# Kernel optimization log

Hardware: AMD Instinct MI355X
Metric: run time of the kernel (lower is better)

Reference implementation:

```python
import jax, jax.numpy as jnp
import numpy as np

B, T, IDIM, ODIM, HDIM = 4, 64, 64, 64, 64
THETAS = np.linspace(0.8, 1.2, 5)


def _argaug(x_dis, y):
    """Grid search over scale thetas and all time shifts; keep best cosine-sim window.
    x_dis: (B,T,H,O) key; y: (B,T,idim) query. Returns (x_aug:(B,T,H,idim), sim:(B,T,H))."""
    Bq, Tq, H, O = x_dis.shape
    idim = y.shape[-1]
    qnorm = jnp.linalg.norm(y, axis=-1)  # (B,T)
    best_sim = None
    best_win = None
    for theta in THETAS:
        L = int(np.floor(O * theta))
        # torch F.interpolate mode='nearest': src = floor(dst * in/out)
        src = np.floor(np.arange(L) * (O / L)).astype(np.int32)
        src = np.clip(src, 0, O - 1)
        x_s = x_dis[..., src]  # (B,T,H,L)
        pad = idim - 1
        xp = jnp.pad(x_s, ((0, 0), (0, 0), (0, 0), (pad, pad)))
        S = L + idim - 1  # number of shifts kept by _pad_for_shift
        win_idx = np.arange(S)[:, None] + np.arange(idim)[None, :]  # (S, idim)
        windows = xp[..., win_idx]  # (B,T,H,S,idim)
        dots = jnp.einsum('bthsi,bti->bths', windows, y)
        wnorm = jnp.linalg.norm(windows, axis=-1)  # (B,T,H,S)
        denom = qnorm[:, :, None, None] * wnorm
        safe = jnp.where(denom > 0, denom, 1.0)
        sim = jnp.where(denom > 0, dots / safe, 0.0)  # nan (0/0) -> 0 as in torch
        sim_max = jnp.max(sim, axis=-1)               # (B,T,H)
        idxm = jnp.argmax(sim, axis=-1)               # first max, like torch.max
        opt = jnp.take_along_axis(windows, idxm[..., None, None], axis=3)[..., 0, :]
        if best_sim is None:
            best_sim, best_win = sim_max, opt
        else:
            m = best_sim < sim_max
            best_win = jnp.where(m[..., None], opt, best_win)
            best_sim = jnp.where(m, sim_max, best_sim)
    return best_win, best_sim


def setup_inputs() -> dict:
    key = jax.random.key(0)
    ks = jax.random.split(key, 6)
    x = jax.random.normal(ks[0], (B, T, IDIM), dtype=jnp.float32)
    y = jax.random.normal(ks[1], (B, T, IDIM), dtype=jnp.float32)
    # freq_mask: Bernoulli per hdim channel with Gaussian-kernel prob (sigma=430)
    w = np.exp(-0.5 * (np.arange(HDIM, dtype=np.float32) / 430.0) ** 2)
    w = w / w.max()
    mask = (jax.random.uniform(ks[2], (B, T, HDIM)) < jnp.asarray(w)).astype(jnp.int32)
    xav = 0.1
    W1 = jax.random.normal(ks[3], (HDIM, IDIM), dtype=jnp.float32) * xav
    W2 = jax.random.normal(ks[4], (ODIM, HDIM), dtype=jnp.float32) * xav
    b1 = jnp.zeros((HDIM,), dtype=jnp.float32)
    b2 = jnp.zeros((ODIM,), dtype=jnp.float32)
    return {"x": x, "y": y, "mask": mask, "W1": W1, "b1": b1, "W2": W2, "b2": b2}


def reference(x, y, mask, W1, b1, W2, b2):
    # h = fc1(x) * mask
    h = jnp.einsum('bti,hi->bth', x, W1) + b1
    h = h * mask.astype(h.dtype)
    # disentangle: fc2(eye*h) -> per-channel rank-1 outputs (B,T,H,O)
    x_dis = jnp.einsum('bth,oh->btho', h, W2) + b2
    # argaug grid search
    x_aug, sim_max_global = _argaug(x_dis, y)  # (B,T,H,idim)
    # h = fc1(x_aug); out = sum_H fc2(h)
    h2 = jnp.einsum('bthi,ji->bthj', x_aug, W1) + b1
    out = jnp.einsum('bthj,oj->btho', h2, W2) + b2
    out = jnp.sum(out, axis=-2)  # (B,T,O)
    xf = out.reshape(-1, out.shape[-1])
    yf = y.reshape(-1, y.shape[-1])
    m = yf == 0.0  # ignore_out = 0.0 (not NaN)
    denom = jnp.sum(~m).astype(xf.dtype)
    loss = jnp.sum(jnp.where(m, 0.0, (xf - yf) ** 2)) / denom
    return loss, xf
```

## Files before the change

### kernel.cpp

```cpp
#include <hip/hip_runtime.h>
#include <math.h>

#define NT 512
#define NWAVE 8

__global__ __launch_bounds__(NT) void argaug_scan(
    const float* __restrict__ x, const float* __restrict__ y,
    const int* __restrict__ mask,
    const float* __restrict__ W1, const float* __restrict__ b1,
    const float* __restrict__ W2, const float* __restrict__ b2,
    double* __restrict__ outN, double* __restrict__ outD, int* __restrict__ outS)
{
    __shared__ double wdBuf[76 * 64];
    __shared__ double ypad[80];
    __shared__ float  sx[64], sh[64], sb1[64];

    double* rsimN = wdBuf;
    double* rsimD = wdBuf + NWAVE * 64;
    int*    ridxB = (int*)(wdBuf + 2 * NWAVE * 64);

    const int tid = threadIdx.x;
    const int bx  = blockIdx.x;
    const int bt  = bx & 255;
    const int t5  = bx >> 8;
    const int hh  = tid & 63;
    const int sg  = tid >> 6;

    const double theta = (t5 == 4) ? 1.2 : (0.8 + (double)t5 * ((1.2 - 0.8) / 4.0));
    const int L = (int)floor(64.0 * theta);
    const int S = L + 63;
    const double rcp = 64.0 / (double)L;

    if (tid < 64) {
        sx[tid]  = x[bt * 64 + tid];
        sb1[tid] = b1[tid];
    } else if (tid >= 128 && tid < 208) {
        const int p = tid - 128;
        ypad[p] = (p >= 8 && p < 72) ? (double)y[bt * 64 + p - 8] : 0.0;
    }
    __syncthreads();

    if (tid < 64) {
        float acc = 0.0f;
        const float* w1r = W1 + tid * 64;
        for (int i = 0; i < 64; ++i) acc = fmaf(sx[i], w1r[i], acc);
        acc += sb1[tid];
        sh[tid] = acc * (float)mask[bt * 64 + tid];
    }
    __syncthreads();

    for (int k = tid; k < L * 64; k += NT) {
        const int j = k >> 6, h = k & 63;
        int sj = (int)floor((double)j * rcp);
        if (sj > 63) sj = 63;
        const float wf = fmaf(sh[h], W2[sj * 64 + h], b2[sj]);
        wdBuf[k] = (double)wf;
    }
    __syncthreads();

    double bN = -1.0, bD = 0.0; int bi = 0x7fffffff;
    #pragma unroll 2
    for (int pp = 0; pp < 2; ++pp) {
        const int s_first = 9 * (sg + 8 * pp);
        if (s_first >= S) continue;
        const int jstart = (s_first > 63) ? (s_first - 63) : 0;
        const int jmid   = (s_first < L - 1) ? s_first : (L - 1);
        const int jend   = (s_first + 8 < L - 1) ? (s_first + 8) : (L - 1);
        const int C      = 71 - s_first;

        double d0=0,d1=0,d2=0,d3=0,d4=0,d5=0,d6=0,d7=0,d8=0,ssA=0;
        double ym1 = ypad[jstart + C - 1];
        double ym2 = ypad[jstart + C - 2];
        double ym3 = ypad[jstart + C - 3];
        double ym4 = ypad[jstart + C - 4];
        double ym5 = ypad[jstart + C - 5];
        double ym6 = ypad[jstart + C - 6];
        double ym7 = ypad[jstart + C - 7];
        double ym8 = ypad[jstart + C - 8];

        #pragma unroll 9
        for (int j = jstart; j <= jmid; ++j) {
            const double w  = wdBuf[j * 64 + hh];
            const double y0 = ypad[j + C];
            d0 = fma(w, y0,  d0); d1 = fma(w, ym1, d1); d2 = fma(w, ym2, d2);
            d3 = fma(w, ym3, d3); d4 = fma(w, ym4, d4); d5 = fma(w, ym5, d5);
            d6 = fma(w, ym6, d6); d7 = fma(w, ym7, d7); d8 = fma(w, ym8, d8);
            ssA = fma(w, w, ssA);
            ym8=ym7; ym7=ym6; ym6=ym5; ym5=ym4; ym4=ym3; ym3=ym2; ym2=ym1; ym1=y0;
        }
        #pragma unroll 9
        for (int j = jmid + 1; j <= jend; ++j) {
            const double w  = wdBuf[j * 64 + hh];
            const double y0 = ypad[j + C];
            d0 = fma(w, y0,  d0); d1 = fma(w, ym1, d1); d2 = fma(w, ym2, d2);
            d3 = fma(w, ym3, d3); d4 = fma(w, ym4, d4); d5 = fma(w, ym5, d5);
            d6 = fma(w, ym6, d6); d7 = fma(w, ym7, d7); d8 = fma(w, ym8, d8);
            ym8=ym7; ym7=ym6; ym6=ym5; ym5=ym4; ym4=ym3; ym3=ym2; ym2=ym1; ym1=y0;
        }

        const int kmax = (S - s_first < 9) ? (S - s_first) : 9;
        double ss = ssA;
        #define SSUP(kk) { \
            const int jh = s_first + kk; \
            const int jl = jh - 64; \
            if (jh <= L - 1) { const double w = wdBuf[jh * 64 + hh]; ss = fma(w,  w, ss); } \
            if (jl >= 0)     { const double w = wdBuf[jl * 64 + hh]; ss = fma(-w, w, ss); } }
        #define EVALK(kk, dk) { \
            double pn, pd; \
            if (ss > 0.0) { pn = dk * fabs(dk); pd = ss; } \
            else          { pn = 0.0;           pd = 1.0; } \
            if (pn * bD > bN * pd) { bN = pn; bD = pd; bi = s_first + kk; } }
        EVALK(0, d0)
        if (1 < kmax) { SSUP(1) EVALK(1, d1) }
        if (2 < kmax) { SSUP(2) EVALK(2, d2) }
        if (3 < kmax) { SSUP(3) EVALK(3, d3) }
        if (4 < kmax) { SSUP(4) EVALK(4, d4) }
        if (5 < kmax) { SSUP(5) EVALK(5, d5) }
        if (6 < kmax) { SSUP(6) EVALK(6, d6) }
        if (7 < kmax) { SSUP(7) EVALK(7, d7) }
        if (8 < kmax) { SSUP(8) EVALK(8, d8) }
        #undef SSUP
        #undef EVALK
    }

    __syncthreads();
    rsimN[sg * 64 + hh] = bN;
    rsimD[sg * 64 + hh] = bD;
    ridxB[sg * 64 + hh] = bi;
    __syncthreads();
    if (tid < 64) {
        double mN = -1.0, mD = 0.0; int mi = 0x7fffffff;
        for (int g = 0; g < NWAVE; ++g) {
            const double vN = rsimN[g * 64 + tid];
            const double vD = rsimD[g * 64 + tid];
            const int    vi = ridxB[g * 64 + tid];
            const double a = vN * mD, b = mN * vD;
            if (a > b || (a == b && vi < mi)) { mN = vN; mD = vD; mi = vi; }
        }
        const int o = bx * 64 + tid;
        outN[o] = mN;
        outD[o] = mD;
        outS[o] = mi;
    }
}

__global__ __launch_bounds__(256) void merge_epilogue(
    const float* __restrict__ x, const float* __restrict__ y,
    const int* __restrict__ mask,
    const float* __restrict__ W1, const float* __restrict__ b1,
    const float* __restrict__ W2, const float* __restrict__ b2,
    const double* __restrict__ N, const double* __restrict__ D,
    const int* __restrict__ S,
    float* __restrict__ xf, double* __restrict__ psum, double* __restrict__ pcnt)
{
    __shared__ float  sx[64], sy[64], sh[64];
    __shared__ int    bS[64], bT[64];
    __shared__ double part[4][64], ssum[64], su[64];

    const int tid = threadIdx.x;
    const int bt  = blockIdx.x;
    const int g   = tid >> 6, i = tid & 63;

    if (tid < 64) {
        sx[tid] = x[bt * 64 + tid];
        sy[tid] = y[bt * 64 + tid];
    }
    __syncthreads();
    if (tid < 64) {
        float acc = 0.0f;
        const float* w1r = W1 + tid * 64;
        for (int k = 0; k < 64; ++k) acc = fmaf(sx[k], w1r[k], acc);
        acc += b1[tid];
        sh[tid] = acc * (float)mask[bt * 64 + tid];
        double mN = -1.0, mD = 0.0; int mS = 0, mT = 0;
        for (int t5 = 0; t5 < 5; ++t5) {
            const int o = (t5 * 256 + bt) * 64 + tid;
            const double vN = N[o], vD = D[o];
            if (vN * mD > mN * vD) { mN = vN; mD = vD; mS = S[o]; mT = t5; }
        }
        bS[tid] = mS; bT[tid] = mT;
    }
    __syncthreads();

    {
        double acc = 0.0;
        for (int q = 0; q < 16; ++q) {
            const int h = g * 16 + q;
            const int t5 = bT[h];
            const double theta = (t5 == 4) ? 1.2 : (0.8 + (double)t5 * ((1.2 - 0.8) / 4.0));
            const int L = (int)floor(64.0 * theta);
            const double rcp = 64.0 / (double)L;
            const int j = bS[h] - 63 + i;
            if (j >= 0 && j < L) {
                int sj = (int)floor((double)j * rcp);
                if (sj > 63) sj = 63;
                acc += (double)fmaf(sh[h], W2[sj * 64 + h], b2[sj]);
            }
        }
        part[g][i] = acc;
    }
    __syncthreads();
    if (tid < 64) {
        ssum[tid] = part[0][tid] + part[1][tid] + part[2][tid] + part[3][tid];
    }
    __syncthreads();
    {
        double acc = 0.0;
        const int base = g * 16;
        for (int q = 0; q < 16; ++q)
            acc += (double)W1[i * 64 + base + q] * ssum[base + q];
        part[g][i] = acc;
    }
    __syncthreads();
    if (tid < 64) {
        su[tid] = 64.0 * (double)b1[tid]
                + part[0][tid] + part[1][tid] + part[2][tid] + part[3][tid];
    }
    __syncthreads();
    {
        double acc = 0.0;
        const int base = g * 16;
        for (int q = 0; q < 16; ++q)
            acc += (double)W2[i * 64 + base + q] * su[base + q];
        part[g][i] = acc;
    }
    __syncthreads();
    if (tid < 64) {
        const double v = 64.0 * (double)b2[tid]
                       + part[0][tid] + part[1][tid] + part[2][tid] + part[3][tid];
        const float outf = (float)v;
        xf[bt * 64 + tid] = outf;
        const float yv = sy[tid];
        double pl = 0.0, pc = 0.0;
        if (yv != 0.0f) {
            const float d = outf - yv;
            pl = (double)(d * d);
            pc = 1.0;
        }
        for (int o = 32; o > 0; o >>= 1) {
            pl += __shfl_down(pl, o, 64);
            pc += __shfl_down(pc, o, 64);
        }
        if (tid == 0) { psum[bt] = pl; pcnt[bt] = pc; }
    }
}

__global__ __launch_bounds__(256) void finalize_loss(
    const double* __restrict__ psum, const double* __restrict__ pcnt,
    float* __restrict__ out)
{
    __shared__ double a[256], c[256];
    const int t = threadIdx.x;
    a[t] = psum[t];
    c[t] = pcnt[t];
    __syncthreads();
    for (int s = 128; s > 0; s >>= 1) {
        if (t < s) { a[t] += a[t + s]; c[t] += c[t + s]; }
        __syncthreads();
    }
    if (t == 0) out[0] = (float)(a[0] / c[0]);
}

extern "C" void kernel_launch(void* const* d_in, const int* in_sizes, int n_in,
                              void* d_out, int out_size, void* d_ws, size_t ws_size,
                              hipStream_t stream) {
    const float* x    = (const float*)d_in[0];
    const float* y    = (const float*)d_in[1];
    const int*   mask = (const int*)d_in[2];
    const float* W1   = (const float*)d_in[3];
    const float* b1   = (const float*)d_in[4];
    const float* W2   = (const float*)d_in[5];
    const float* b2   = (const float*)d_in[6];
    float* out = (float*)d_out;

    char* ws = (char*)d_ws;
    double* Nw   = (double*)(ws);
    double* Dw   = (double*)(ws + 655360);
    int*    Sw   = (int*)(ws + 1310720);
    double* psum = (double*)(ws + 1638400);
    double* pcnt = (double*)(ws + 1640448);

    argaug_scan<<<1280, NT, 0, stream>>>(x, y, mask, W1, b1, W2, b2,
                                         Nw, Dw, Sw);
    merge_epilogue<<<256, 256, 0, stream>>>(x, y, mask, W1, b1, W2, b2,
                                            Nw, Dw, Sw,
                                            out + 1, psum, pcnt);
    finalize_loss<<<1, 256, 0, stream>>>(psum, pcnt, out);
}
```

Before: 49.80 us.

## Fuse scan, merge and loss into one kernel with last-block atomic counters

Merges the three kernels into a single launch. Per-(b,t) atomic counters let the last of the five theta blocks run the merge and epilogue, and a global counter lets the last block reduce the loss. Similarity is stored as one quotient instead of a numerator/denominator pair, and the inner loop is rewritten with register rotation macros instead of shift chains. Block-to-(bt,theta) mapping becomes interleaved. It adds a memset launch and atomics/threadfences, and storing the quotient may change tie-breaking slightly.

Measured after the change: 81.91 us. 1.64x slower.

```diff
diff --git a/kernel.cpp b/kernel.cpp
--- a/kernel.cpp
+++ b/kernel.cpp
@@ -2,27 +2,64 @@
 #include <math.h>
 
 #define NT 512
-#define NWAVE 8
-
-__global__ __launch_bounds__(NT) void argaug_scan(
+
+#define BODYS(J, R0,R1,R2,R3,R4,R5,R6,R7,R8) { \
+    const double wv = wdBuf[(J) * 64 + hh]; \
+    R0 = ypad[(J) + C]; \
+    d0 = fma(wv, R0, d0); d1 = fma(wv, R1, d1); d2 = fma(wv, R2, d2); \
+    d3 = fma(wv, R3, d3); d4 = fma(wv, R4, d4); d5 = fma(wv, R5, d5); \
+    d6 = fma(wv, R6, d6); d7 = fma(wv, R7, d7); d8 = fma(wv, R8, d8); \
+    ssq = fma(wv, wv, ssq); }
+
+#define BODYN(J, R0,R1,R2,R3,R4,R5,R6,R7,R8) { \
+    const double wv = wdBuf[(J) * 64 + hh]; \
+    R0 = ypad[(J) + C]; \
+    d0 = fma(wv, R0, d0); d1 = fma(wv, R1, d1); d2 = fma(wv, R2, d2); \
+    d3 = fma(wv, R3, d3); d4 = fma(wv, R4, d4); d5 = fma(wv, R5, d5); \
+    d6 = fma(wv, R6, d6); d7 = fma(wv, R7, d7); d8 = fma(wv, R8, d8); }
+
+#define BS(J, R) BODYS(J, R)
+#define BN(J, R) BODYN(J, R)
+
+#define ROT0 q0,q1,q2,q3,q4,q5,q6,q7,q8
+#define ROT1 q8,q0,q1,q2,q3,q4,q5,q6,q7
+#define ROT2 q7,q8,q0,q1,q2,q3,q4,q5,q6
+#define ROT3 q6,q7,q8,q0,q1,q2,q3,q4,q5
+#define ROT4 q5,q6,q7,q8,q0,q1,q2,q3,q4
+#define ROT5 q4,q5,q6,q7,q8,q0,q1,q2,q3
+#define ROT6 q3,q4,q5,q6,q7,q8,q0,q1,q2
+#define ROT7 q2,q3,q4,q5,q6,q7,q8,q0,q1
+#define ROT8 q1,q2,q3,q4,q5,q6,q7,q8,q0
+
+#define PROLOG(JB) { \
+    q1 = ypad[(JB) + C - 1]; q2 = ypad[(JB) + C - 2]; \
+    q3 = ypad[(JB) + C - 3]; q4 = ypad[(JB) + C - 4]; \
+    q5 = ypad[(JB) + C - 5]; q6 = ypad[(JB) + C - 6]; \
+    q7 = ypad[(JB) + C - 7]; q8 = ypad[(JB) + C - 8]; }
+
+__global__ __launch_bounds__(NT) void argaug_fused(
     const float* __restrict__ x, const float* __restrict__ y,
     const int* __restrict__ mask,
     const float* __restrict__ W1, const float* __restrict__ b1,
     const float* __restrict__ W2, const float* __restrict__ b2,
-    double* __restrict__ outN, double* __restrict__ outD, int* __restrict__ outS)
+    double* __restrict__ simW, int* __restrict__ SwG,
+    double* __restrict__ psum, double* __restrict__ pcnt,
+    int* __restrict__ cnt_bt, int* __restrict__ cnt_all,
+    float* out)
 {
     __shared__ double wdBuf[76 * 64];
     __shared__ double ypad[80];
-    __shared__ float  sx[64], sh[64], sb1[64];
-
-    double* rsimN = wdBuf;
-    double* rsimD = wdBuf + NWAVE * 64;
-    int*    ridxB = (int*)(wdBuf + 2 * NWAVE * 64);
+    __shared__ float  sxy[64];
+    __shared__ float  sh[64], sb1[64];
+    __shared__ int    eflag[2];
+
+    double* rsimQ = wdBuf;
+    int*    ridxB = (int*)(wdBuf + 512);
 
     const int tid = threadIdx.x;
     const int bx  = blockIdx.x;
-    const int bt  = bx & 255;
-    const int t5  = bx >> 8;
+    const int bt  = bx / 5;
+    const int t5  = bx % 5;
     const int hh  = tid & 63;
     const int sg  = tid >> 6;
 
@@ -32,7 +69,7 @@
     const double rcp = 64.0 / (double)L;
 
     if (tid < 64) {
-        sx[tid]  = x[bt * 64 + tid];
+        sxy[tid] = x[bt * 64 + tid];
         sb1[tid] = b1[tid];
     } else if (tid >= 128 && tid < 208) {
         const int p = tid - 128;
@@ -43,7 +80,7 @@
     if (tid < 64) {
         float acc = 0.0f;
         const float* w1r = W1 + tid * 64;
-        for (int i = 0; i < 64; ++i) acc = fmaf(sx[i], w1r[i], acc);
+        for (int i = 0; i < 64; ++i) acc = fmaf(sxy[i], w1r[i], acc);
         acc += sb1[tid];
         sh[tid] = acc * (float)mask[bt * 64 + tid];
     }
@@ -53,13 +90,12 @@
         const int j = k >> 6, h = k & 63;
         int sj = (int)floor((double)j * rcp);
         if (sj > 63) sj = 63;
-        const float wf = fmaf(sh[h], W2[sj * 64 + h], b2[sj]);
-        wdBuf[k] = (double)wf;
+        wdBuf[k] = (double)fmaf(sh[h], W2[sj * 64 + h], b2[sj]);
     }
     __syncthreads();
 
     double bN = -1.0, bD = 0.0; int bi = 0x7fffffff;
-    #pragma unroll 2
+    #pragma unroll 1
     for (int pp = 0; pp < 2; ++pp) {
         const int s_first = 9 * (sg + 8 * pp);
         if (s_first >= S) continue;
@@ -68,38 +104,44 @@
         const int jend   = (s_first + 8 < L - 1) ? (s_first + 8) : (L - 1);
         const int C      = 71 - s_first;
 
-        double d0=0,d1=0,d2=0,d3=0,d4=0,d5=0,d6=0,d7=0,d8=0,ssA=0;
-        double ym1 = ypad[jstart + C - 1];
-        double ym2 = ypad[jstart + C - 2];
-        double ym3 = ypad[jstart + C - 3];
-        double ym4 = ypad[jstart + C - 4];
-        double ym5 = ypad[jstart + C - 5];
-        double ym6 = ypad[jstart + C - 6];
-        double ym7 = ypad[jstart + C - 7];
-        double ym8 = ypad[jstart + C - 8];
-
-        #pragma unroll 9
-        for (int j = jstart; j <= jmid; ++j) {
-            const double w  = wdBuf[j * 64 + hh];
-            const double y0 = ypad[j + C];
-            d0 = fma(w, y0,  d0); d1 = fma(w, ym1, d1); d2 = fma(w, ym2, d2);
-            d3 = fma(w, ym3, d3); d4 = fma(w, ym4, d4); d5 = fma(w, ym5, d5);
-            d6 = fma(w, ym6, d6); d7 = fma(w, ym7, d7); d8 = fma(w, ym8, d8);
-            ssA = fma(w, w, ssA);
-            ym8=ym7; ym7=ym6; ym6=ym5; ym5=ym4; ym4=ym3; ym3=ym2; ym2=ym1; ym1=y0;
-        }
-        #pragma unroll 9
-        for (int j = jmid + 1; j <= jend; ++j) {
-            const double w  = wdBuf[j * 64 + hh];
-            const double y0 = ypad[j + C];
-            d0 = fma(w, y0,  d0); d1 = fma(w, ym1, d1); d2 = fma(w, ym2, d2);
-            d3 = fma(w, ym3, d3); d4 = fma(w, ym4, d4); d5 = fma(w, ym5, d5);
-            d6 = fma(w, ym6, d6); d7 = fma(w, ym7, d7); d8 = fma(w, ym8, d8);
-            ym8=ym7; ym7=ym6; ym6=ym5; ym5=ym4; ym4=ym3; ym3=ym2; ym2=ym1; ym1=y0;
+        double d0=0,d1=0,d2=0,d3=0,d4=0,d5=0,d6=0,d7=0,d8=0,ssq=0;
+        double q0=0,q1,q2,q3,q4,q5,q6,q7,q8;
+
+        int j = jstart;
+        PROLOG(j)
+        const int endA = jmid + 1;
+        while (j + 9 <= endA) {
+            BS(j+0, ROT0) BS(j+1, ROT1) BS(j+2, ROT2)
+            BS(j+3, ROT3) BS(j+4, ROT4) BS(j+5, ROT5)
+            BS(j+6, ROT6) BS(j+7, ROT7) BS(j+8, ROT8)
+            j += 9;
+        }
+        const int remA = endA - j;
+        if (remA > 0) { BS(j+0, ROT0) }
+        if (remA > 1) { BS(j+1, ROT1) }
+        if (remA > 2) { BS(j+2, ROT2) }
+        if (remA > 3) { BS(j+3, ROT3) }
+        if (remA > 4) { BS(j+4, ROT4) }
+        if (remA > 5) { BS(j+5, ROT5) }
+        if (remA > 6) { BS(j+6, ROT6) }
+        if (remA > 7) { BS(j+7, ROT7) }
+
+        const int lenB = jend - jmid;
+        if (lenB > 0) {
+            j = jmid + 1;
+            PROLOG(j)
+            { BN(j+0, ROT0) }
+            if (lenB > 1) { BN(j+1, ROT1) }
+            if (lenB > 2) { BN(j+2, ROT2) }
+            if (lenB > 3) { BN(j+3, ROT3) }
+            if (lenB > 4) { BN(j+4, ROT4) }
+            if (lenB > 5) { BN(j+5, ROT5) }
+            if (lenB > 6) { BN(j+6, ROT6) }
+            if (lenB > 7) { BN(j+7, ROT7) }
         }
 
         const int kmax = (S - s_first < 9) ? (S - s_first) : 9;
-        double ss = ssA;
+        double ss = ssq;
         #define SSUP(kk) { \
             const int jh = s_first + kk; \
             const int jl = jh - 64; \
@@ -124,113 +166,101 @@
     }
 
     __syncthreads();
-    rsimN[sg * 64 + hh] = bN;
-    rsimD[sg * 64 + hh] = bD;
+    rsimQ[sg * 64 + hh] = bN / bD;
     ridxB[sg * 64 + hh] = bi;
     __syncthreads();
     if (tid < 64) {
-        double mN = -1.0, mD = 0.0; int mi = 0x7fffffff;
-        for (int g = 0; g < NWAVE; ++g) {
-            const double vN = rsimN[g * 64 + tid];
-            const double vD = rsimD[g * 64 + tid];
-            const int    vi = ridxB[g * 64 + tid];
-            const double a = vN * mD, b = mN * vD;
-            if (a > b || (a == b && vi < mi)) { mN = vN; mD = vD; mi = vi; }
-        }
-        const int o = bx * 64 + tid;
-        outN[o] = mN;
-        outD[o] = mD;
-        outS[o] = mi;
-    }
-}
-
-__global__ __launch_bounds__(256) void merge_epilogue(
-    const float* __restrict__ x, const float* __restrict__ y,
-    const int* __restrict__ mask,
-    const float* __restrict__ W1, const float* __restrict__ b1,
-    const float* __restrict__ W2, const float* __restrict__ b2,
-    const double* __restrict__ N, const double* __restrict__ D,
-    const int* __restrict__ S,
-    float* __restrict__ xf, double* __restrict__ psum, double* __restrict__ pcnt)
-{
-    __shared__ float  sx[64], sy[64], sh[64];
-    __shared__ int    bS[64], bT[64];
-    __shared__ double part[4][64], ssum[64], su[64];
-
-    const int tid = threadIdx.x;
-    const int bt  = blockIdx.x;
-    const int g   = tid >> 6, i = tid & 63;
-
-    if (tid < 64) {
-        sx[tid] = x[bt * 64 + tid];
-        sy[tid] = y[bt * 64 + tid];
-    }
-    __syncthreads();
-    if (tid < 64) {
-        float acc = 0.0f;
-        const float* w1r = W1 + tid * 64;
-        for (int k = 0; k < 64; ++k) acc = fmaf(sx[k], w1r[k], acc);
-        acc += b1[tid];
-        sh[tid] = acc * (float)mask[bt * 64 + tid];
-        double mN = -1.0, mD = 0.0; int mS = 0, mT = 0;
-        for (int t5 = 0; t5 < 5; ++t5) {
-            const int o = (t5 * 256 + bt) * 64 + tid;
-            const double vN = N[o], vD = D[o];
-            if (vN * mD > mN * vD) { mN = vN; mD = vD; mS = S[o]; mT = t5; }
-        }
-        bS[tid] = mS; bT[tid] = mT;
+        double m = rsimQ[tid]; int mi = ridxB[tid];
+        for (int g = 1; g < 8; ++g) {
+            const double v = rsimQ[g * 64 + tid]; const int vi = ridxB[g * 64 + tid];
+            if (v > m || (v == m && vi < mi)) { m = v; mi = vi; }
+        }
+        const int o = (t5 * 256 + bt) * 64 + tid;
+        simW[o] = m;
+        SwG[o]  = mi;
+    }
+    __syncthreads();
+
+    if (tid == 0) {
+        __threadfence();
+        const int old = atomicAdd(&cnt_bt[bt], 1);
+        if (old == 4) { __threadfence(); eflag[0] = 1; } else eflag[0] = 0;
+    }
+    __syncthreads();
+    if (eflag[0] == 0) return;
+
+    double* mpart = wdBuf;
+    double* mssum = wdBuf + 512;
+    double* msu   = wdBuf + 576;
+    int*    mbS   = (int*)(wdBuf + 640);
+    int*    mbT   = mbS + 64;
+
+    if (tid < 64) {
+        sxy[tid] = y[bt * 64 + tid];
+        int o0 = bt * 64 + tid;
+        double mN = simW[o0]; int mS = SwG[o0], mT = 0;
+        for (int t = 1; t < 5; ++t) {
+            const int o = (t * 256 + bt) * 64 + tid;
+            const double v = simW[o];
+            if (v > mN) { mN = v; mS = SwG[o]; mT = t; }
+        }
+        mbS[tid] = mS; mbT[tid] = mT;
     }
     __syncthreads();
 
     {
+        const int g = sg, i = hh;
         double acc = 0.0;
-        for (int q = 0; q < 16; ++q) {
-            const int h = g * 16 + q;
-            const int t5 = bT[h];
-            const double theta = (t5 == 4) ? 1.2 : (0.8 + (double)t5 * ((1.2 - 0.8) / 4.0));
-            const int L = (int)floor(64.0 * theta);
-            const double rcp = 64.0 / (double)L;
-            const int j = bS[h] - 63 + i;
-            if (j >= 0 && j < L) {
-                int sj = (int)floor((double)j * rcp);
+        for (int q = 0; q < 8; ++q) {
+            const int h = g * 8 + q;
+            const int t = mbT[h];
+            const double th2 = (t == 4) ? 1.2 : (0.8 + (double)t * ((1.2 - 0.8) / 4.0));
+            const int Lh = (int)floor(64.0 * th2);
+            const double rc = 64.0 / (double)Lh;
+            const int jj = mbS[h] - 63 + i;
+            if (jj >= 0 && jj < Lh) {
+                int sj = (int)floor((double)jj * rc);
                 if (sj > 63) sj = 63;
                 acc += (double)fmaf(sh[h], W2[sj * 64 + h], b2[sj]);
             }
         }
-        part[g][i] = acc;
-    }
-    __syncthreads();
-    if (tid < 64) {
-        ssum[tid] = part[0][tid] + part[1][tid] + part[2][tid] + part[3][tid];
+        mpart[g * 64 + i] = acc;
+    }
+    __syncthreads();
+    if (tid < 64) {
+        double s0 = 0.0;
+        for (int g = 0; g < 8; ++g) s0 += mpart[g * 64 + tid];
+        mssum[tid] = s0;
     }
     __syncthreads();
     {
+        const int g = sg, i = hh, base = g * 8;
         double acc = 0.0;
-        const int base = g * 16;
-        for (int q = 0; q < 16; ++q)
-            acc += (double)W1[i * 64 + base + q] * ssum[base + q];
-        part[g][i] = acc;
-    }
-    __syncthreads();
-    if (tid < 64) {
-        su[tid] = 64.0 * (double)b1[tid]
-                + part[0][tid] + part[1][tid] + part[2][tid] + part[3][tid];
+        for (int q = 0; q < 8; ++q)
+            acc += (double)W1[i * 64 + base + q] * mssum[base + q];
+        mpart[g * 64 + i] = acc;
+    }
+    __syncthreads();
+    if (tid < 64) {
+        double s0 = 64.0 * (double)sb1[tid];
+        for (int g = 0; g < 8; ++g) s0 += mpart[g * 64 + tid];
+        msu[tid] = s0;
     }
     __syncthreads();
     {
+        const int g = sg, i = hh, base = g * 8;
         double acc = 0.0;
-        const int base = g * 16;
-        for (int q = 0; q < 16; ++q)
-            acc += (double)W2[i * 64 + base + q] * su[base + q];
-        part[g][i] = acc;
-    }
-    __syncthreads();
-    if (tid < 64) {
-        const double v = 64.0 * (double)b2[tid]
-                       + part[0][tid] + part[1][tid] + part[2][tid] + part[3][tid];
+        for (int q = 0; q < 8; ++q)
+            acc += (double)W2[i * 64 + base + q] * msu[base + q];
+        mpart[g * 64 + i] = acc;
+    }
+    __syncthreads();
+    if (tid < 64) {
+        double v = 64.0 * (double)b2[tid];
+        for (int g = 0; g < 8; ++g) v += mpart[g * 64 + tid];
         const float outf = (float)v;
-        xf[bt * 64 + tid] = outf;
-        const float yv = sy[tid];
+        out[1 + bt * 64 + tid] = outf;
+        const float yv = sxy[tid];
         double pl = 0.0, pc = 0.0;
         if (yv != 0.0f) {
             const float d = outf - yv;
@@ -243,22 +273,28 @@
         }
         if (tid == 0) { psum[bt] = pl; pcnt[bt] = pc; }
     }
-}
-
-__global__ __launch_bounds__(256) void finalize_loss(
-    const double* __restrict__ psum, const double* __restrict__ pcnt,
-    float* __restrict__ out)
-{
-    __shared__ double a[256], c[256];
-    const int t = threadIdx.x;
-    a[t] = psum[t];
-    c[t] = pcnt[t];
-    __syncthreads();
-    for (int s = 128; s > 0; s >>= 1) {
-        if (t < s) { a[t] += a[t + s]; c[t] += c[t + s]; }
-        __syncthreads();
-    }
-    if (t == 0) out[0] = (float)(a[0] / c[0]);
+    __syncthreads();
+
+    if (tid == 0) {
+        __threadfence();
+        const int old = atomicAdd(cnt_all, 1);
+        if (old == 255) { __threadfence(); eflag[1] = 1; } else eflag[1] = 0;
+    }
+    __syncthreads();
+    if (eflag[1] == 0) return;
+
+    if (tid < 64) {
+        double a = 0.0, c = 0.0;
+        for (int r = 0; r < 4; ++r) {
+            a += psum[tid * 4 + r];
+            c += pcnt[tid * 4 + r];
+        }
+        for (int o = 32; o > 0; o >>= 1) {
+            a += __shfl_down(a, o, 64);
+            c += __shfl_down(c, o, 64);
+        }
+        if (tid == 0) out[0] = (float)(a / c);
+    }
 }
 
 extern "C" void kernel_launch(void* const* d_in, const int* in_sizes, int n_in,
@@ -274,16 +310,15 @@
     float* out = (float*)d_out;
 
     char* ws = (char*)d_ws;
-    double* Nw   = (double*)(ws);
-    double* Dw   = (double*)(ws + 655360);
-    int*    Sw   = (int*)(ws + 1310720);
-    double* psum = (double*)(ws + 1638400);
-    double* pcnt = (double*)(ws + 1640448);
-
-    argaug_scan<<<1280, NT, 0, stream>>>(x, y, mask, W1, b1, W2, b2,
-                                         Nw, Dw, Sw);
-    merge_epilogue<<<256, 256, 0, stream>>>(x, y, mask, W1, b1, W2, b2,
-                                            Nw, Dw, Sw,
-                                            out + 1, psum, pcnt);
-    finalize_loss<<<1, 256, 0, stream>>>(psum, pcnt, out);
+    double* simW   = (double*)(ws);
+    int*    SwG    = (int*)(ws + 655360);
+    double* psum   = (double*)(ws + 983040);
+    double* pcnt   = (double*)(ws + 985088);
+    int*    cnt_bt = (int*)(ws + 987136);
+    int*    cnt_all= cnt_bt + 256;
+
+    hipMemsetAsync(ws + 987136, 0, 257 * sizeof(int), stream);
+    argaug_fused<<<1280, NT, 0, stream>>>(x, y, mask, W1, b1, W2, b2,
+                                          simW, SwG, psum, pcnt,
+                                          cnt_bt, cnt_all, out);
 }
```
